# Performance work log

Measured on AMD Instinct MI355X. Metric: run time of the kernel, lower is better.

Reference implementation:

```python
import jax, jax.numpy as jnp
import numpy as np
import math

LN_EPS = 1e-5

def _ln(x, g, b):
    m = jnp.mean(x, -1, keepdims=True)
    v = jnp.mean((x - m) ** 2, -1, keepdims=True)
    return (x - m) / jnp.sqrt(v + LN_EPS) * g + b

def setup_inputs() -> dict:
    key = jax.random.key(0)
    ks = jax.random.split(key, 16)
    B, N, D, V = 2, 512, 128, 16
    w = lambda k, shape: jax.random.normal(k, shape, jnp.float32) * 0.02
    return {
        "scalar": jax.random.normal(ks[0], (B, N, D), jnp.float32),
        "vector": jax.random.normal(ks[1], (B, N, 3, V), jnp.float32),
        "coords": jax.random.normal(ks[2], (B, N, 3), jnp.float32),
        "w_q": w(ks[3], (D, D)), "b_q": jnp.zeros((D,), jnp.float32),
        "w_k": w(ks[4], (D, D)), "b_k": jnp.zeros((D,), jnp.float32),
        "w_v": w(ks[5], (D, D)), "b_v": jnp.zeros((D,), jnp.float32),
        "w_d1": w(ks[6], (1, D)), "b_d1": jnp.zeros((D,), jnp.float32),
        "w_d2": w(ks[7], (D, D)), "b_d2": jnp.zeros((D,), jnp.float32),
        "w_g": w(ks[8], (D, V)), "b_g": jnp.zeros((V,), jnp.float32),
        "w_o": w(ks[9], (D, D)), "b_o": jnp.zeros((D,), jnp.float32),
        "w_f1": w(ks[10], (D, 2 * D)), "b_f1": jnp.zeros((2 * D,), jnp.float32),
        "w_f2": w(ks[11], (2 * D, D)), "b_f2": jnp.zeros((D,), jnp.float32),
        "w_vo": w(ks[12], (V, V)), "b_vo": jnp.zeros((V,), jnp.float32),
        "g_s": jnp.ones((D,), jnp.float32), "be_s": jnp.zeros((D,), jnp.float32),
        "g_v": jnp.ones((V,), jnp.float32), "be_v": jnp.zeros((V,), jnp.float32),
    }

def reference(scalar, vector, coords, w_q, b_q, w_k, b_k, w_v, b_v,
              w_d1, b_d1, w_d2, b_d2, w_g, b_g, w_o, b_o,
              w_f1, b_f1, w_f2, b_f2, w_vo, b_vo, g_s, be_s, g_v, be_v):
    D = scalar.shape[-1]
    # pairwise geometry: [B,N,N,3], [B,N,N,1]
    rel = coords[:, :, None, :] - coords[:, None, :, :]
    dist = jnp.linalg.norm(rel, axis=-1, keepdims=True)
    direction = rel / jnp.maximum(dist, 1e-6)
    sn = _ln(scalar, g_s, be_s)
    q = sn @ w_q + b_q
    k = sn @ w_k + b_k
    v = sn @ w_v + b_v
    # distance-conditioned bias: [B,N,N,D]
    bias = jax.nn.gelu(dist @ w_d1 + b_d1, approximate=False) @ w_d2 + b_d2
    # q_i . (k_j + bias_ij) / sqrt(D)
    logits = (jnp.einsum('bid,bjd->bij', q, k)
              + jnp.einsum('bid,bijd->bij', q, bias)) / math.sqrt(D)
    attn = jax.nn.softmax(logits, axis=-1)
    # sum_j attn_ij * (v_j + bias_ij)
    upd = jnp.einsum('bij,bjd->bid', attn, v) + jnp.einsum('bij,bijd->bid', attn, bias)
    scalar = scalar + (upd @ w_o + b_o)
    h = _ln(scalar, g_s, be_s)
    scalar = scalar + (jax.nn.gelu(h @ w_f1 + b_f1, approximate=False) @ w_f2 + b_f2)
    gate = jax.nn.sigmoid(scalar @ w_g + b_g)  # [B,N,V]
    # sum_j attn_ij * (vector_j + dir_ij * gate_i) decomposed (same math, no BxNxNx3xV tensor)
    agg = (jnp.einsum('bij,bjcv->bicv', attn, vector)
           + jnp.einsum('bij,bijc->bic', attn, direction)[..., None] * gate[:, :, None, :])
    projected = _ln(agg, g_v, be_v) @ w_vo + b_vo
    return scalar, vector + projected
```

## Files before the change

kernel.cpp:

```cpp
#include <hip/hip_runtime.h>
#include <math.h>

#define D 128
#define F 256
#define V 16
#define NSEQ 512
#define NROW 1024
#define MQ 7

__device__ __forceinline__ float gelu_exact(float x) {
    return 0.5f * x * (1.0f + erff(x * 0.70710678118654752f));
}

__device__ __forceinline__ float waveSum(float v) {
#pragma unroll
    for (int o = 32; o; o >>= 1) v += __shfl_xor(v, o);
    return v;
}
__device__ __forceinline__ float waveMax(float v) {
#pragma unroll
    for (int o = 32; o; o >>= 1) v = fmaxf(v, __shfl_xor(v, o));
    return v;
}

__device__ __forceinline__ void build_A(const float* __restrict__ w_d1,
                                        const float* __restrict__ b_d1,
                                        float* A_s, int t) {
    if (t < D) {
        const float gam[MQ] = {0.f, 0.5f, 0.39894228f, 0.f, -0.06649038f, 0.f,
                               0.0099735570f};
        float w = w_d1[t], b = b_d1[t];
        float wp[MQ], bp[MQ];
        wp[0] = 1.f; bp[0] = 1.f;
#pragma unroll
        for (int i = 1; i < MQ; i++) { wp[i] = wp[i - 1] * w; bp[i] = bp[i - 1] * b; }
        float A[MQ];
#pragma unroll
        for (int m = 0; m < MQ; m++) A[m] = 0.f;
#pragma unroll
        for (int k = 1; k < MQ; k++) {
            float g = gam[k];
            if (g == 0.f) continue;
            float C = 1.f;
            for (int m = 0; m <= k; m++) {
                A[m] = fmaf(g * C, wp[m] * bp[k - m], A[m]);
                C = C * (float)(k - m) / (float)(m + 1);
            }
        }
#pragma unroll
        for (int m = 0; m < MQ; m++) A_s[t * MQ + m] = A[m];
    }
}

__global__ __launch_bounds__(1024, 8) void k1_qkv(
    const float* __restrict__ scalar,
    const float* __restrict__ w_q, const float* __restrict__ b_q,
    const float* __restrict__ w_k, const float* __restrict__ b_k,
    const float* __restrict__ w_v, const float* __restrict__ b_v,
    const float* __restrict__ w_d1, const float* __restrict__ b_d1,
    const float* __restrict__ w_d2,
    const float* __restrict__ g_s, const float* __restrict__ be_s,
    float* __restrict__ qg, float* __restrict__ kTg, float* __restrict__ vg,
    float* __restrict__ Gg)
{
    const int t = threadIdx.x, l = t & 127, h2 = (t >> 7) & 1;
    const int wvid = t >> 6, ln = t & 63;
    const int r0 = blockIdx.x * 2, r = r0 + h2;
    __shared__ __align__(8) float snT[D][2];
    __shared__ float k_s[2][D];
    __shared__ float A_s[D * MQ];
    __shared__ float P3[3][8][2][D];
    __shared__ float redA[16], redB[16];

    float x = scalar[(size_t)r * D + l];
    { float s = waveSum(x); if (ln == 0) redA[wvid] = s; }
    __syncthreads();
    float mean = 0.f;
#pragma unroll
    for (int dd = 0; dd < 4; dd++) mean += redA[4 * dd + 2 * h2] + redA[4 * dd + 2 * h2 + 1];
    mean *= (1.0f / 512.0f);
    float dv = x - mean;
    { float s = waveSum(dv * dv); if (ln == 0) redB[wvid] = s; }
    __syncthreads();
    float var = 0.f;
#pragma unroll
    for (int dd = 0; dd < 4; dd++) var += redB[4 * dd + 2 * h2] + redB[4 * dd + 2 * h2 + 1];
    var *= (1.0f / 512.0f);
    if (t < 256) snT[l][h2] = dv * rsqrtf(var + 1e-5f) * g_s[l] + be_s[l];
    __syncthreads();

    {
        const int eo = t >> 7, e0 = eo * 16;
        float aq0 = 0.f, aq1 = 0.f, ak0 = 0.f, ak1 = 0.f, av0 = 0.f, av1 = 0.f;
#pragma unroll 4
        for (int e = e0; e < e0 + 16; e++) {
            float2 s2 = *(const float2*)&snT[e][0];
            float wq = w_q[e * D + l], wk = w_k[e * D + l], wv = w_v[e * D + l];
            aq0 = fmaf(s2.x, wq, aq0); aq1 = fmaf(s2.y, wq, aq1);
            ak0 = fmaf(s2.x, wk, ak0); ak1 = fmaf(s2.y, wk, ak1);
            av0 = fmaf(s2.x, wv, av0); av1 = fmaf(s2.y, wv, av1);
        }
        P3[0][eo][0][l] = aq0; P3[0][eo][1][l] = aq1;
        P3[1][eo][0][l] = ak0; P3[1][eo][1][l] = ak1;
        P3[2][eo][0][l] = av0; P3[2][eo][1][l] = av1;
    }
    __syncthreads();

    if (t < 768) {
        const int mat = t >> 8, h3 = (t >> 7) & 1, l2 = t & 127;
        float acc = 0.f;
#pragma unroll
        for (int eo = 0; eo < 8; eo++) acc += P3[mat][eo][h3][l2];
        if (mat == 0)      qg[(size_t)(r0 + h3) * D + l2] = acc + b_q[l2];
        else if (mat == 1) k_s[h3][l2] = acc + b_k[l2];
        else               vg[(size_t)(r0 + h3) * D + l2] = acc + b_v[l2];
    }
    __syncthreads();
    if (t < 256) kTg[(size_t)(t >> 1) * NROW + r0 + (t & 1)] = k_s[t & 1][t >> 1];

    if (blockIdx.x == 0) {
        build_A(w_d1, b_d1, A_s, t);
        __syncthreads();
        if (t < D * MQ) {
            const int m = t >> 7, l2 = t & 127;
            float acc = 0.f;
#pragma unroll 4
            for (int e = 0; e < D; e++)
                acc = fmaf(w_d2[e * D + l2], A_s[e * MQ + m], acc);
            Gg[l2 * MQ + m] = acc;
        }
    }
}

__global__ __launch_bounds__(1024, 8) void k23(
    const float* __restrict__ coords, const float* __restrict__ vecin,
    const float* __restrict__ scalar,
    const float* __restrict__ qg, const float* __restrict__ kTg,
    const float* __restrict__ vg, const float* __restrict__ Gg,
    const float* __restrict__ b_d2,
    const float* __restrict__ w_o, const float* __restrict__ b_o,
    const float* __restrict__ w_f1, const float* __restrict__ b_f1,
    const float* __restrict__ w_f2, const float* __restrict__ b_f2,
    const float* __restrict__ w_g, const float* __restrict__ b_g,
    const float* __restrict__ w_vo, const float* __restrict__ b_vo,
    const float* __restrict__ g_s, const float* __restrict__ be_s,
    const float* __restrict__ g_v, const float* __restrict__ be_v,
    float* __restrict__ out_s, float* __restrict__ out_v)
{
    const int t = threadIdx.x, wvid = t >> 6, ln = t & 63;
    const int r0 = blockIdx.x * 2, b = blockIdx.x >> 8;
    __shared__ __align__(16) float RA[10752];
    __shared__ __align__(8) float qT[D][2];
    __shared__ float Gl[D * MQ];
    __shared__ float P_s[2][MQ];
    __shared__ __align__(8) float updT[D][2], hT[D][2], s1T[D][2];
    __shared__ __align__(8) float t2T[F][2];
    __shared__ float S_s[2][MQ], adir_s[2][3], avec_s[2][48];
    __shared__ float redA[16], redB[16], wredM[16][10];
    __shared__ float gate_s[2][V], gp[8][2][V], lnv_s[2][48];

    if (t < 256) qT[t & 127][t >> 7] = qg[(size_t)(r0 + (t >> 7)) * D + (t & 127)];
    if (t < D * MQ) Gl[t] = Gg[t];
    __syncthreads();

    {
        const int dd = t & 127, h2 = (t >> 7) & 1;
        float qv = qT[dd][h2];
        float pa[MQ];
#pragma unroll
        for (int m = 0; m < MQ; m++) pa[m] = qv * Gl[dd * MQ + m];
        pa[0] = fmaf(qv, b_d2[dd], pa[0]);
#pragma unroll
        for (int m = 0; m < MQ; m++) {
            float s = waveSum(pa[m]);
            if (ln == 0) wredM[wvid][m] = s;
        }
    }
    __syncthreads();
    if (t < 2 * MQ) {
        const int hh = t / MQ, m = t % MQ;
        float s = 0.f;
#pragma unroll
        for (int dd = 0; dd < 4; dd++)
            s += wredM[4 * dd + 2 * hh][m] + wredM[4 * dd + 2 * hh + 1][m];
        P_s[hh][m] = s * 0.25f;
    }

    {
        const int jq = t & 127, j0 = jq * 4, eq = t >> 7, e0 = eq * 16;
        const float* ke = kTg + (size_t)e0 * NROW + (size_t)b * NSEQ + j0;
        float c00 = 0.f, c01 = 0.f, c02 = 0.f, c03 = 0.f;
        float c10 = 0.f, c11 = 0.f, c12 = 0.f, c13 = 0.f;
#pragma unroll 4
        for (int e = 0; e < 16; e++) {
            float4 kv = *(const float4*)&ke[(size_t)e * NROW];
            float2 q2 = *(const float2*)&qT[e0 + e][0];
            c00 = fmaf(q2.x, kv.x, c00); c01 = fmaf(q2.x, kv.y, c01);
            c02 = fmaf(q2.x, kv.z, c02); c03 = fmaf(q2.x, kv.w, c03);
            c10 = fmaf(q2.y, kv.x, c10); c11 = fmaf(q2.y, kv.y, c11);
            c12 = fmaf(q2.y, kv.z, c12); c13 = fmaf(q2.y, kv.w, c13);
        }
        *(float4*)&RA[1024 + (eq * 2 + 0) * 512 + j0] = make_float4(c00, c01, c02, c03);
        *(float4*)&RA[1024 + (eq * 2 + 1) * 512 + j0] = make_float4(c10, c11, c12, c13);
    }
    __syncthreads();

    const int h2 = t >> 9, j = t & 511, r = r0 + h2;
    const float cix = coords[(size_t)r * 3 + 0];
    const float ciy = coords[(size_t)r * 3 + 1];
    const float ciz = coords[(size_t)r * 3 + 2];
    const float* cj = coords + ((size_t)b * NSEQ + j) * 3;
    float rx = cix - cj[0], ry = ciy - cj[1], rz = ciz - cj[2];
    float dj = sqrtf(rx * rx + ry * ry + rz * rz);
    float qk = 0.f;
#pragma unroll
    for (int eq = 0; eq < 8; eq++) qk += RA[1024 + (eq * 2 + h2) * 512 + j];
    float Pr[MQ];
#pragma unroll
    for (int m = 0; m < MQ; m++) Pr[m] = P_s[h2][m];
    float bias = Pr[MQ - 1];
#pragma unroll
    for (int m = MQ - 2; m >= 0; m--) bias = fmaf(bias, dj, Pr[m]);
    const float sc = 0.08838834764831844f;
    float lg = (qk + bias) * sc;

    { float mx = waveMax(lg); if (ln == 0) redA[wvid] = mx; }
    __syncthreads();
    float mx = redA[8 * h2];
#pragma unroll
    for (int k = 1; k < 8; k++) mx = fmaxf(mx, redA[8 * h2 + k]);
    float p = __expf(lg - mx);
    { float s = waveSum(p); if (ln == 0) redB[wvid] = s; }
    __syncthreads();
    float lsum = 0.f;
#pragma unroll
    for (int k = 0; k < 8; k++) lsum += redB[8 * h2 + k];
    float a = p / lsum;
    RA[j * 2 + h2] = a;

    {
        float red[10];
        float w0 = a;
#pragma unroll
        for (int m = 0; m < MQ; m++) { red[m] = w0; w0 *= dj; }
        float ia = a * __builtin_amdgcn_rcpf(fmaxf(dj, 1e-6f));
        red[7] = ia * rx; red[8] = ia * ry; red[9] = ia * rz;
#pragma unroll
        for (int m = 0; m < 10; m++) {
            float s = waveSum(red[m]);
            if (ln == 0) wredM[wvid][m] = s;
        }
    }
    __syncthreads();
    if (t < 20) {
        const int hh = t / 10, m = t % 10;
        float s = 0.f;
#pragma unroll
        for (int k = 0; k < 8; k++) s += wredM[8 * hh + k][m];
        if (m < MQ) S_s[hh][m] = s;
        else        adir_s[hh][m - MQ] = s;
    }

    {
        const int dq = t & 31, d0 = dq * 4, jo = t >> 5, jb = 16 * jo;
        const float* vb = vg + ((size_t)b * NSEQ + jb) * D + d0;
        float c00 = 0.f, c01 = 0.f, c02 = 0.f, c03 = 0.f;
        float c10 = 0.f, c11 = 0.f, c12 = 0.f, c13 = 0.f;
#pragma unroll 4
        for (int jj = 0; jj < 16; jj++) {
            float2 at = *(const float2*)&RA[(jb + jj) * 2];
            float4 vv = *(const float4*)&vb[(size_t)jj * D];
            c00 = fmaf(at.x, vv.x, c00); c01 = fmaf(at.x, vv.y, c01);
            c02 = fmaf(at.x, vv.z, c02); c03 = fmaf(at.x, vv.w, c03);
            c10 = fmaf(at.y, vv.x, c10); c11 = fmaf(at.y, vv.y, c11);
            c12 = fmaf(at.y, vv.z, c12); c13 = fmaf(at.y, vv.w, c13);
        }
        *(float4*)&RA[1024 + (jo * 2 + 0) * 128 + d0] = make_float4(c00, c01, c02, c03);
        *(float4*)&RA[1024 + (jo * 2 + 1) * 128 + d0] = make_float4(c10, c11, c12, c13);
    }
    if (ln < 48) {
        const int jb = 32 * wvid;
        const float* vp = vecin + ((size_t)b * NSEQ + jb) * 48 + ln;
        float c0 = 0.f, c1 = 0.f;
#pragma unroll 4
        for (int jj = 0; jj < 32; jj++) {
            float2 at = *(const float2*)&RA[(jb + jj) * 2];
            float vv = vp[(size_t)jj * 48];
            c0 = fmaf(at.x, vv, c0);
            c1 = fmaf(at.y, vv, c1);
        }
        RA[9216 + (wvid * 2 + 0) * 48 + ln] = c0;
        RA[9216 + (wvid * 2 + 1) * 48 + ln] = c1;
    }
    __syncthreads();

    if (t < 256) {
        const int hh = t >> 7, l = t & 127;
        float acc = 0.f;
#pragma unroll
        for (int jo = 0; jo < 32; jo++) acc += RA[1024 + (jo * 2 + hh) * 128 + l];
        float aa = 0.f;
#pragma unroll
        for (int m = 0; m < MQ; m++) aa = fmaf(Gl[l * MQ + m], S_s[hh][m], aa);
        updT[l][hh] = acc + aa + b_d2[l];
    } else if (t - 256 < 96) {
        const int idx = t - 256, hh = idx / 48, i2 = idx % 48;
        float s = 0.f;
#pragma unroll
        for (int w2 = 0; w2 < 16; w2++) s += RA[9216 + (w2 * 2 + hh) * 48 + i2];
        avec_s[hh][i2] = s;
    }
    __syncthreads();

    {
        const int eo = t >> 7, l = t & 127, e0 = 16 * eo;
        float c0 = 0.f, c1 = 0.f;
#pragma unroll 4
        for (int e = e0; e < e0 + 16; e++) {
            float2 up = *(const float2*)&updT[e][0];
            float wv = w_o[e * D + l];
            c0 = fmaf(up.x, wv, c0);
            c1 = fmaf(up.y, wv, c1);
        }
        RA[2048 + (eo * 2 + 0) * 128 + l] = c0;
        RA[2048 + (eo * 2 + 1) * 128 + l] = c1;
    }
    __syncthreads();
    float xln = 0.f;
    {
        const int hh = (t >> 7) & 1, l = t & 127;
        if (t < 256) {
            float acc = 0.f;
#pragma unroll
            for (int eo = 0; eo < 8; eo++) acc += RA[2048 + (eo * 2 + hh) * 128 + l];
            xln = scalar[(size_t)(r0 + hh) * D + l] + acc + b_o[l];
            s1T[l][hh] = xln;
        }
        float s = waveSum(xln);
        if (t < 256 && ln == 0) redA[wvid] = s;
    }
    __syncthreads();
    float dvv = 0.f;
    if (t < 256) {
        const int hh = (t >> 7) & 1;
        float mean = (redA[2 * hh] + redA[2 * hh + 1]) * (1.0f / 128.0f);
        dvv = xln - mean;
    }
    {
        float s = waveSum(dvv * dvv);
        if (t < 256 && ln == 0) redB[wvid] = s;
    }
    __syncthreads();
    if (t < 256) {
        const int hh = (t >> 7) & 1, l = t & 127;
        float var = (redB[2 * hh] + redB[2 * hh + 1]) * (1.0f / 128.0f);
        hT[l][hh] = dvv * rsqrtf(var + 1e-5f) * g_s[l] + be_s[l];
    }
    __syncthreads();

    {
        const int f = t & 255, eq = t >> 8, e0 = 32 * eq;
        float c0 = 0.f, c1 = 0.f;
#pragma unroll 4
        for (int e = e0; e < e0 + 32; e++) {
            float2 hv = *(const float2*)&hT[e][0];
            float wv = w_f1[e * F + f];
            c0 = fmaf(hv.x, wv, c0);
            c1 = fmaf(hv.y, wv, c1);
        }
        RA[2048 + (eq * 2 + 0) * 256 + f] = c0;
        RA[2048 + (eq * 2 + 1) * 256 + f] = c1;
    }
    __syncthreads();
    if (t < 512) {
        const int hh = t >> 8, f = t & 255;
        float acc = 0.f;
#pragma unroll
        for (int eq = 0; eq < 4; eq++) acc += RA[2048 + (eq * 2 + hh) * 256 + f];
        t2T[f][hh] = gelu_exact(acc + b_f1[f]);
    }
    __syncthreads();

    {
        const int fo = t >> 7, l = t & 127, f0 = 32 * fo;
        float c0 = 0.f, c1 = 0.f;
#pragma unroll 4
        for (int f = f0; f < f0 + 32; f++) {
            float2 tv = *(const float2*)&t2T[f][0];
            float wv = w_f2[f * D + l];
            c0 = fmaf(tv.x, wv, c0);
            c1 = fmaf(tv.y, wv, c1);
        }
        RA[2048 + (fo * 2 + 0) * 128 + l] = c0;
        RA[2048 + (fo * 2 + 1) * 128 + l] = c1;
    }
    __syncthreads();
    if (t < 256) {
        const int hh = t >> 7, l = t & 127;
        float acc = 0.f;
#pragma unroll
        for (int fo = 0; fo < 8; fo++) acc += RA[2048 + (fo * 2 + hh) * 128 + l];
        float v2 = s1T[l][hh] + acc + b_f2[l];
        out_s[(size_t)(r0 + hh) * D + l] = v2;
        s1T[l][hh] = v2;
    }
    __syncthreads();

    if (t < 256) {
        const int dq = t >> 5, rr = (t >> 4) & 1, vv = t & 15, d0 = 16 * dq;
        float aa = 0.f;
#pragma unroll 4
        for (int dd = d0; dd < d0 + 16; dd++)
            aa = fmaf(s1T[dd][rr], w_g[dd * V + vv], aa);
        gp[dq][rr][vv] = aa;
    }
    __syncthreads();
    if (t < 32) {
        const int rr = t >> 4, vv = t & 15;
        float aa = b_g[vv];
#pragma unroll
        for (int dq = 0; dq < 8; dq++) aa += gp[dq][rr][vv];
        gate_s[rr][vv] = 1.0f / (1.0f + __expf(-aa));
    }
    __syncthreads();

    if (t < 96) {
        const int rr = t / 48, idx = t % 48, c = idx >> 4, vv = idx & 15;
        float agg = avec_s[rr][idx] + adir_s[rr][c] * gate_s[rr][vv];
        float s = agg;
#pragma unroll
        for (int o = 8; o; o >>= 1) s += __shfl_xor(s, o, 16);
        float mean = s * (1.0f / 16.0f);
        float e = agg - mean;
        float s2 = e * e;
#pragma unroll
        for (int o = 8; o; o >>= 1) s2 += __shfl_xor(s2, o, 16);
        float rstd = rsqrtf(s2 * (1.0f / 16.0f) + 1e-5f);
        lnv_s[rr][idx] = e * rstd * g_v[vv] + be_v[vv];
    }
    __syncthreads();
    if (t < 96) {
        const int rr = t / 48, idx = t % 48, c = idx >> 4, vv = idx & 15;
        const int row = r0 + rr;
        float aa = b_vo[vv];
#pragma unroll
        for (int w2 = 0; w2 < V; w2++)
            aa = fmaf(lnv_s[rr][c * V + w2], w_vo[w2 * V + vv], aa);
        out_v[(size_t)row * 48 + idx] = vecin[(size_t)row * 48 + idx] + aa;
    }
}

extern "C" void kernel_launch(void* const* d_in, const int* in_sizes, int n_in,
                              void* d_out, int out_size, void* d_ws, size_t ws_size,
                              hipStream_t stream)
{
    (void)in_sizes; (void)n_in; (void)out_size; (void)ws_size;
    const float* scalar = (const float*)d_in[0];
    const float* vecin  = (const float*)d_in[1];
    const float* coords = (const float*)d_in[2];
    const float* w_q  = (const float*)d_in[3];  const float* b_q  = (const float*)d_in[4];
    const float* w_k  = (const float*)d_in[5];  const float* b_k  = (const float*)d_in[6];
    const float* w_v  = (const float*)d_in[7];  const float* b_v  = (const float*)d_in[8];
    const float* w_d1 = (const float*)d_in[9];  const float* b_d1 = (const float*)d_in[10];
    const float* w_d2 = (const float*)d_in[11]; const float* b_d2 = (const float*)d_in[12];
    const float* w_g  = (const float*)d_in[13]; const float* b_g  = (const float*)d_in[14];
    const float* w_o  = (const float*)d_in[15]; const float* b_o  = (const float*)d_in[16];
    const float* w_f1 = (const float*)d_in[17]; const float* b_f1 = (const float*)d_in[18];
    const float* w_f2 = (const float*)d_in[19]; const float* b_f2 = (const float*)d_in[20];
    const float* w_vo = (const float*)d_in[21]; const float* b_vo = (const float*)d_in[22];
    const float* g_s  = (const float*)d_in[23]; const float* be_s = (const float*)d_in[24];
    const float* g_v  = (const float*)d_in[25]; const float* be_v = (const float*)d_in[26];

    float* ws  = (float*)d_ws;
    float* qg  = ws;
    float* kTg = ws + 131072;
    float* vg  = ws + 262144;
    float* Gg  = ws + 393216;

    float* out_s = (float*)d_out;
    float* out_v = out_s + 131072;

    hipLaunchKernelGGL(k1_qkv, dim3(NROW / 2), dim3(1024), 0, stream,
                       scalar, w_q, b_q, w_k, b_k, w_v, b_v, w_d1, b_d1,
                       w_d2, g_s, be_s, qg, kTg, vg, Gg);
    hipLaunchKernelGGL(k23, dim3(NROW / 2), dim3(1024), 0, stream,
                       coords, vecin, scalar, qg, kTg, vg, Gg,
                       b_d2, w_o, b_o, w_f1, b_f1, w_f2, b_f2,
                       w_g, b_g, w_vo, b_vo, g_s, be_s, g_v, be_v,
                       out_s, out_v);
}
```

Before: 158.5 us.

## Fuse QKV projection and attention kernels with a software grid barrier

Merges the two kernels into one persistent launch. The QKV/LayerNorm stage writes K and V to global memory, then all blocks meet at an atomic-counter grid barrier before the attention stage. Q stays in shared memory rather than round-tripping through global. This removes one kernel launch and the gap between launches. The cost is a memset per call and a spin barrier that depends on all 512 blocks of 1024 threads being resident at once; if they are not, the kernel deadlocks.

```diff
diff --git a/kernel.cpp b/kernel.cpp
--- a/kernel.cpp
+++ b/kernel.cpp
@@ -52,92 +52,14 @@
     }
 }
 
-__global__ __launch_bounds__(1024, 8) void k1_qkv(
-    const float* __restrict__ scalar,
+__global__ __launch_bounds__(1024, 8) void fused(
+    const float* __restrict__ scalar, const float* __restrict__ vecin,
+    const float* __restrict__ coords,
     const float* __restrict__ w_q, const float* __restrict__ b_q,
     const float* __restrict__ w_k, const float* __restrict__ b_k,
     const float* __restrict__ w_v, const float* __restrict__ b_v,
     const float* __restrict__ w_d1, const float* __restrict__ b_d1,
-    const float* __restrict__ w_d2,
-    const float* __restrict__ g_s, const float* __restrict__ be_s,
-    float* __restrict__ qg, float* __restrict__ kTg, float* __restrict__ vg,
-    float* __restrict__ Gg)
-{
-    const int t = threadIdx.x, l = t & 127, h2 = (t >> 7) & 1;
-    const int wvid = t >> 6, ln = t & 63;
-    const int r0 = blockIdx.x * 2, r = r0 + h2;
-    __shared__ __align__(8) float snT[D][2];
-    __shared__ float k_s[2][D];
-    __shared__ float A_s[D * MQ];
-    __shared__ float P3[3][8][2][D];
-    __shared__ float redA[16], redB[16];
-
-    float x = scalar[(size_t)r * D + l];
-    { float s = waveSum(x); if (ln == 0) redA[wvid] = s; }
-    __syncthreads();
-    float mean = 0.f;
-#pragma unroll
-    for (int dd = 0; dd < 4; dd++) mean += redA[4 * dd + 2 * h2] + redA[4 * dd + 2 * h2 + 1];
-    mean *= (1.0f / 512.0f);
-    float dv = x - mean;
-    { float s = waveSum(dv * dv); if (ln == 0) redB[wvid] = s; }
-    __syncthreads();
-    float var = 0.f;
-#pragma unroll
-    for (int dd = 0; dd < 4; dd++) var += redB[4 * dd + 2 * h2] + redB[4 * dd + 2 * h2 + 1];
-    var *= (1.0f / 512.0f);
-    if (t < 256) snT[l][h2] = dv * rsqrtf(var + 1e-5f) * g_s[l] + be_s[l];
-    __syncthreads();
-
-    {
-        const int eo = t >> 7, e0 = eo * 16;
-        float aq0 = 0.f, aq1 = 0.f, ak0 = 0.f, ak1 = 0.f, av0 = 0.f, av1 = 0.f;
-#pragma unroll 4
-        for (int e = e0; e < e0 + 16; e++) {
-            float2 s2 = *(const float2*)&snT[e][0];
-            float wq = w_q[e * D + l], wk = w_k[e * D + l], wv = w_v[e * D + l];
-            aq0 = fmaf(s2.x, wq, aq0); aq1 = fmaf(s2.y, wq, aq1);
-            ak0 = fmaf(s2.x, wk, ak0); ak1 = fmaf(s2.y, wk, ak1);
-            av0 = fmaf(s2.x, wv, av0); av1 = fmaf(s2.y, wv, av1);
-        }
-        P3[0][eo][0][l] = aq0; P3[0][eo][1][l] = aq1;
-        P3[1][eo][0][l] = ak0; P3[1][eo][1][l] = ak1;
-        P3[2][eo][0][l] = av0; P3[2][eo][1][l] = av1;
-    }
-    __syncthreads();
-
-    if (t < 768) {
-        const int mat = t >> 8, h3 = (t >> 7) & 1, l2 = t & 127;
-        float acc = 0.f;
-#pragma unroll
-        for (int eo = 0; eo < 8; eo++) acc += P3[mat][eo][h3][l2];
-        if (mat == 0)      qg[(size_t)(r0 + h3) * D + l2] = acc + b_q[l2];
-        else if (mat == 1) k_s[h3][l2] = acc + b_k[l2];
-        else               vg[(size_t)(r0 + h3) * D + l2] = acc + b_v[l2];
-    }
-    __syncthreads();
-    if (t < 256) kTg[(size_t)(t >> 1) * NROW + r0 + (t & 1)] = k_s[t & 1][t >> 1];
-
-    if (blockIdx.x == 0) {
-        build_A(w_d1, b_d1, A_s, t);
-        __syncthreads();
-        if (t < D * MQ) {
-            const int m = t >> 7, l2 = t & 127;
-            float acc = 0.f;
-#pragma unroll 4
-            for (int e = 0; e < D; e++)
-                acc = fmaf(w_d2[e * D + l2], A_s[e * MQ + m], acc);
-            Gg[l2 * MQ + m] = acc;
-        }
-    }
-}
-
-__global__ __launch_bounds__(1024, 8) void k23(
-    const float* __restrict__ coords, const float* __restrict__ vecin,
-    const float* __restrict__ scalar,
-    const float* __restrict__ qg, const float* __restrict__ kTg,
-    const float* __restrict__ vg, const float* __restrict__ Gg,
-    const float* __restrict__ b_d2,
+    const float* __restrict__ w_d2, const float* __restrict__ b_d2,
     const float* __restrict__ w_o, const float* __restrict__ b_o,
     const float* __restrict__ w_f1, const float* __restrict__ b_f1,
     const float* __restrict__ w_f2, const float* __restrict__ b_f2,
@@ -145,6 +67,8 @@
     const float* __restrict__ w_vo, const float* __restrict__ b_vo,
     const float* __restrict__ g_s, const float* __restrict__ be_s,
     const float* __restrict__ g_v, const float* __restrict__ be_v,
+    float* __restrict__ kTg, float* __restrict__ vg, float* __restrict__ Gg,
+    unsigned int* __restrict__ bar,
     float* __restrict__ out_s, float* __restrict__ out_v)
 {
     const int t = threadIdx.x, wvid = t >> 6, ln = t & 63;
@@ -159,7 +83,88 @@
     __shared__ float redA[16], redB[16], wredM[16][10];
     __shared__ float gate_s[2][V], gp[8][2][V], lnv_s[2][48];
 
-    if (t < 256) qT[t & 127][t >> 7] = qg[(size_t)(r0 + (t >> 7)) * D + (t & 127)];
+    {
+        float* snT1 = RA;
+        float* k_s1 = RA + 256;
+        float* A_s1 = RA + 512;
+        float* P31  = RA + 1408;
+
+        const int l = t & 127, hh = (t >> 7) & 1;
+        const int r = r0 + hh;
+        float x = scalar[(size_t)r * D + l];
+        { float s = waveSum(x); if (ln == 0) redA[wvid] = s; }
+        __syncthreads();
+        float mean = 0.f;
+#pragma unroll
+        for (int dd = 0; dd < 4; dd++) mean += redA[4 * dd + 2 * hh] + redA[4 * dd + 2 * hh + 1];
+        mean *= (1.0f / 512.0f);
+        float dv = x - mean;
+        { float s = waveSum(dv * dv); if (ln == 0) redB[wvid] = s; }
+        __syncthreads();
+        float var = 0.f;
+#pragma unroll
+        for (int dd = 0; dd < 4; dd++) var += redB[4 * dd + 2 * hh] + redB[4 * dd + 2 * hh + 1];
+        var *= (1.0f / 512.0f);
+        if (t < 256) snT1[l * 2 + hh] = dv * rsqrtf(var + 1e-5f) * g_s[l] + be_s[l];
+        __syncthreads();
+
+        {
+            const int eo = t >> 7, e0 = eo * 16;
+            float aq0 = 0.f, aq1 = 0.f, ak0 = 0.f, ak1 = 0.f, av0 = 0.f, av1 = 0.f;
+#pragma unroll 4
+            for (int e = e0; e < e0 + 16; e++) {
+                float2 s2 = *(const float2*)&snT1[e * 2];
+                float wq = w_q[e * D + l], wk = w_k[e * D + l], wv = w_v[e * D + l];
+                aq0 = fmaf(s2.x, wq, aq0); aq1 = fmaf(s2.y, wq, aq1);
+                ak0 = fmaf(s2.x, wk, ak0); ak1 = fmaf(s2.y, wk, ak1);
+                av0 = fmaf(s2.x, wv, av0); av1 = fmaf(s2.y, wv, av1);
+            }
+            P31[((0 * 8 + eo) * 2 + 0) * D + l] = aq0; P31[((0 * 8 + eo) * 2 + 1) * D + l] = aq1;
+            P31[((1 * 8 + eo) * 2 + 0) * D + l] = ak0; P31[((1 * 8 + eo) * 2 + 1) * D + l] = ak1;
+            P31[((2 * 8 + eo) * 2 + 0) * D + l] = av0; P31[((2 * 8 + eo) * 2 + 1) * D + l] = av1;
+        }
+        __syncthreads();
+
+        if (t < 768) {
+            const int mat = t >> 8, h3 = (t >> 7) & 1, l2 = t & 127;
+            float acc = 0.f;
+#pragma unroll
+            for (int eo = 0; eo < 8; eo++) acc += P31[((mat * 8 + eo) * 2 + h3) * D + l2];
+            if (mat == 0)      qT[l2][h3] = acc + b_q[l2];
+            else if (mat == 1) k_s1[h3 * D + l2] = acc + b_k[l2];
+            else               vg[(size_t)(r0 + h3) * D + l2] = acc + b_v[l2];
+        }
+        __syncthreads();
+        if (t < 256) kTg[(size_t)(t >> 1) * NROW + r0 + (t & 1)] = k_s1[(t & 1) * D + (t >> 1)];
+
+        if (blockIdx.x == 0) {
+            build_A(w_d1, b_d1, A_s1, t);
+            __syncthreads();
+            if (t < D * MQ) {
+                const int m = t >> 7, l2 = t & 127;
+                float acc = 0.f;
+#pragma unroll 4
+                for (int e = 0; e < D; e++)
+                    acc = fmaf(w_d2[e * D + l2], A_s1[e * MQ + m], acc);
+                Gg[l2 * MQ + m] = acc;
+            }
+        }
+    }
+
+    __syncthreads();
+    if (t == 0) {
+        __threadfence();
+        unsigned prev = atomicAdd(&bar[0], 1u);
+        if (prev == (unsigned)(gridDim.x - 1)) {
+            __hip_atomic_store(&bar[1], 1u, __ATOMIC_RELEASE, __HIP_MEMORY_SCOPE_AGENT);
+        } else {
+            while (__hip_atomic_load(&bar[1], __ATOMIC_RELAXED, __HIP_MEMORY_SCOPE_AGENT) == 0u)
+                __builtin_amdgcn_s_sleep(2);
+        }
+        __threadfence();
+    }
+    __syncthreads();
+
     if (t < D * MQ) Gl[t] = Gg[t];
     __syncthreads();
 
@@ -472,20 +477,19 @@
     const float* g_v  = (const float*)d_in[25]; const float* be_v = (const float*)d_in[26];
 
     float* ws  = (float*)d_ws;
-    float* qg  = ws;
-    float* kTg = ws + 131072;
-    float* vg  = ws + 262144;
-    float* Gg  = ws + 393216;
+    float* kTg = ws;
+    float* vg  = ws + 131072;
+    float* Gg  = ws + 262144;
+    unsigned int* bar = (unsigned int*)(ws + 263168);
 
     float* out_s = (float*)d_out;
     float* out_v = out_s + 131072;
 
-    hipLaunchKernelGGL(k1_qkv, dim3(NROW / 2), dim3(1024), 0, stream,
-                       scalar, w_q, b_q, w_k, b_k, w_v, b_v, w_d1, b_d1,
-                       w_d2, g_s, be_s, qg, kTg, vg, Gg);
-    hipLaunchKernelGGL(k23, dim3(NROW / 2), dim3(1024), 0, stream,
-                       coords, vecin, scalar, qg, kTg, vg, Gg,
-                       b_d2, w_o, b_o, w_f1, b_f1, w_f2, b_f2,
-                       w_g, b_g, w_vo, b_vo, g_s, be_s, g_v, be_v,
-                       out_s, out_v);
-}
+    hipMemsetAsync(bar, 0, 2 * sizeof(unsigned int), stream);
+    hipLaunchKernelGGL(fused, dim3(NROW / 2), dim3(1024), 0, stream,
+                       scalar, vecin, coords,
+                       w_q, b_q, w_k, b_k, w_v, b_v, w_d1, b_d1, w_d2, b_d2,
+                       w_o, b_o, w_f1, b_f1, w_f2, b_f2, w_g, b_g, w_vo, b_vo,
+                       g_s, be_s, g_v, be_v,
+                       kTg, vg, Gg, bar, out_s, out_v);
+}
```

Result: slower. 207.2 us (+30.7%).
